# Performance work log

Hardware: AMD Instinct MI355X
Metric: run time of the kernel (lower is better)

The kernel has to match this reference:

```python
import jax, jax.numpy as jnp
import numpy as np

EPS = 1e-5


def _gcn_conv(x, src, dst, n_nodes, W, b):
    # x: [N, Fin]; src/dst: [E+N] (self-loops already appended)
    h = x @ W                                   # [N, Fout]
    deg = jnp.zeros((n_nodes,), x.dtype).at[dst].add(1.0)
    dinv = jax.lax.rsqrt(deg)                   # deg >= 1 due to self-loops
    norm = dinv[src] * dinv[dst]                # [E+N]
    msg = h[src] * norm[:, None]                # [E+N, Fout]  (gather)
    out = jax.ops.segment_sum(msg, dst, num_segments=n_nodes)  # scatter-add
    return out + b


def _bn_relu(x, gamma, beta):
    # BatchNorm over nodes (training-style batch statistics), then ReLU.
    mu = jnp.mean(x, axis=0)
    var = jnp.mean((x - mu) ** 2, axis=0)       # biased variance (torch BN)
    xn = (x - mu) * jax.lax.rsqrt(var + EPS)
    return jax.nn.relu(xn * gamma + beta)


def setup_inputs() -> dict:
    key = jax.random.key(0)
    ks = jax.random.split(key, 12)
    N, E, Fin, H, O, G = 100000, 1600000, 128, 128, 64, 128
    x = jax.random.normal(ks[0], (N, Fin), dtype=jnp.float32)
    edge_index = jax.random.randint(ks[1], (2, E), 0, N, dtype=jnp.int64)
    batch = jnp.sort(jax.random.randint(ks[2], (N,), 0, G, dtype=jnp.int64))
    s = 1.0 / np.sqrt(Fin)
    W0 = jax.random.uniform(ks[3], (Fin, H), jnp.float32, -s, s)
    b0 = jnp.zeros((H,), jnp.float32)
    g0 = jnp.ones((H,), jnp.float32)
    be0 = jnp.zeros((H,), jnp.float32)
    s2 = 1.0 / np.sqrt(H)
    W1 = jax.random.uniform(ks[4], (H, H), jnp.float32, -s2, s2)
    b1 = jnp.zeros((H,), jnp.float32)
    g1 = jnp.ones((H,), jnp.float32)
    be1 = jnp.zeros((H,), jnp.float32)
    Wout = jax.random.uniform(ks[5], (H, O), jnp.float32, -s2, s2)
    bout = jax.random.uniform(ks[6], (O,), jnp.float32, -s2, s2)
    return {"x": x, "edge_index": edge_index, "batch": batch, "num_graphs": 128,
            "W0": W0, "b0": b0, "g0": g0, "be0": be0,
            "W1": W1, "b1": b1, "g1": g1, "be1": be1,
            "Wout": Wout, "bout": bout}


def reference(x, edge_index, batch, num_graphs,
              W0, b0, g0, be0, W1, b1, g1, be1, Wout, bout):
    N = x.shape[0]
    loops = jnp.arange(N, dtype=edge_index.dtype)
    src = jnp.concatenate([edge_index[0], loops])  # add self-loops
    dst = jnp.concatenate([edge_index[1], loops])
    h = _gcn_conv(x, src, dst, N, W0, b0)
    h = _bn_relu(h, g0, be0)                       # Dropout(p=0.1) = identity in eval
    h = _gcn_conv(h, src, dst, N, W1, b1)
    h = _bn_relu(h, g1, be1)
    # global mean pool over graphs
    sums = jax.ops.segment_sum(h, batch, num_segments=num_graphs)   # [G, H]
    cnt = jax.ops.segment_sum(jnp.ones((N,), h.dtype), batch, num_segments=num_graphs)
    pooled = sums / jnp.maximum(cnt, 1.0)[:, None]
    return pooled @ Wout + bout
```

## Files before the change

### kernel.cpp

```cpp
#include <hip/hip_runtime.h>
#include <hip/hip_bf16.h>

typedef _Float16 half8_t __attribute__((ext_vector_type(8)));
typedef _Float16 half2_t __attribute__((ext_vector_type(2)));
typedef float float4_t __attribute__((ext_vector_type(4)));
typedef float float2_t __attribute__((ext_vector_type(2)));
typedef unsigned int uint4_t __attribute__((ext_vector_type(4)));


__global__ __launch_bounds__(256) void k_hist(const int* __restrict__ dst, int E, int SH,
                                              int NBK, int WG, int CH, int* __restrict__ M) {
    extern __shared__ int lh[];
    for (int i = threadIdx.x; i < NBK; i += 256) lh[i] = 0;
    __syncthreads();
    int wg = blockIdx.x;
    int e0 = wg * CH, e1 = min(E, e0 + CH);
    for (int e = e0 + threadIdx.x; e < e1; e += 256)
        atomicAdd(&lh[dst[e] >> SH], 1);
    __syncthreads();
    for (int i = threadIdx.x; i < NBK; i += 256) M[i * WG + wg] = lh[i];
}

__global__ __launch_bounds__(256) void k_colscan(int* __restrict__ M, int WG,
                                                 int* __restrict__ totals) {
    __shared__ int s[256];
    int b = blockIdx.x, t = threadIdx.x;
    int v = (t < WG) ? M[b * WG + t] : 0;
    s[t] = v;
    __syncthreads();
    for (int off = 1; off < 256; off <<= 1) {
        int u = (t >= off) ? s[t - off] : 0;
        __syncthreads();
        s[t] += u;
        __syncthreads();
    }
    if (t < WG) M[b * WG + t] = s[t] - v;
    if (t == 255) totals[b] = s[255];
}

__global__ __launch_bounds__(512) void k_bucketscan(const int* __restrict__ totals, int NBK,
                                                    int E, int* __restrict__ base) {
    __shared__ int s[512];
    int t = threadIdx.x;
    int v = (t < NBK) ? totals[t] : 0;
    s[t] = v;
    __syncthreads();
    for (int off = 1; off < 512; off <<= 1) {
        int u = (t >= off) ? s[t - off] : 0;
        __syncthreads();
        s[t] += u;
        __syncthreads();
    }
    if (t < NBK) base[t] = s[t] - v;
    if (t == 0) base[NBK] = E;
}

__global__ __launch_bounds__(256) void k_scatter(const int* __restrict__ src,
                                                 const int* __restrict__ dst, int E, int SH,
                                                 int NBK, int WG, int CH,
                                                 const int* __restrict__ M,
                                                 const int* __restrict__ base,
                                                 unsigned* __restrict__ ebuf) {
    extern __shared__ int cur[];
    int wg = blockIdx.x;
    for (int i = threadIdx.x; i < NBK; i += 256) cur[i] = base[i] + M[i * WG + wg];
    __syncthreads();
    int e0 = wg * CH, e1 = min(E, e0 + CH);
    for (int e = e0 + threadIdx.x; e < e1; e += 256) {
        int d = dst[e];
        int b = d >> SH;
        int pos = atomicAdd(&cur[b], 1);
        ebuf[pos] = (unsigned)src[e] | ((unsigned)(d - (b << SH)) << 23);
    }
}

__global__ __launch_bounds__(256) void k_cntfill(const unsigned* __restrict__ ebuf,
                                                 const int* __restrict__ base, int SH, int N,
                                                 int E, float* __restrict__ dinv,
                                                 int* __restrict__ rp, int* __restrict__ colx,
                                                 int* __restrict__ slots,
                                                 const float* __restrict__ W0,
                                                 const float* __restrict__ W1,
                                                 _Float16* __restrict__ Wt0,
                                                 _Float16* __restrict__ Wt1,
                                                 const int* __restrict__ batch, int G,
                                                 int* __restrict__ gptr,
                                                 float* __restrict__ psum,
                                                 float* __restrict__ sums,
                                                 unsigned char* __restrict__ A8) {
    __shared__ int h[512];
    __shared__ int cur[512];
    __shared__ int rs[512];
    __shared__ int lim[512];
    __shared__ int s[256];
    int b = blockIdx.x, t = threadIdx.x;

    if (b < 64) {
        int idx = b * 256 + t;
        int n = idx >> 7, k = idx & 127;
        Wt0[n * 128 + k] = (_Float16)W0[k * 128 + n];
        Wt1[n * 128 + k] = (_Float16)W1[k * 128 + n];
    } else if (b == 64) {
        if (t <= G) {
            int g = t;
            int lo = 0, hi = N;
            while (lo < hi) {
                int mid = (lo + hi) >> 1;
                if (batch[mid] < g) lo = mid + 1; else hi = mid;
            }
            gptr[g] = lo;
        }
    } else if (b < 97) {
        int i0 = (b - 65) * 512 + t;
        psum[i0] = 0.f;
        psum[i0 + 256] = 0.f;
    } else if (b == 97) {
        if (t < 256) { sums[t] = 0.f; sums[t + 256] = 0.f; }
        if (t < 32) ((unsigned*)A8)[(size_t)N * 32 + t] = 0u;
    }

    int n0 = b << SH;
    int nb = min(N - n0, 1 << SH);
    for (int i = t; i < nb; i += 256) h[i] = 0;
    __syncthreads();
    int e0 = base[b], e1 = base[b + 1];
    for (int e = e0 + t; e < e1; e += 256)
        atomicAdd(&h[ebuf[e] >> 23], 1);
    __syncthreads();
    int i0 = 2 * t, i1 = 2 * t + 1;
    int a0 = (i0 < nb) ? h[i0] : 0;
    int a1 = (i1 < nb) ? h[i1] : 0;
    int ps = a0 + a1;
    s[t] = ps;
    __syncthreads();
    for (int off = 1; off < 256; off <<= 1) {
        int u = (t >= off) ? s[t - off] : 0;
        __syncthreads();
        s[t] += u;
        __syncthreads();
    }
    int excl = s[t] - ps;
    if (i0 < nb) {
        int r0 = e0 + excl;
        cur[i0] = r0;
        rs[i0] = r0;
        lim[i0] = min(a0, 32);
        rp[n0 + i0] = r0;
        dinv[n0 + i0] = rsqrtf((float)(a0 + 1));
    }
    if (i1 < nb) {
        int r1 = e0 + excl + a0;
        cur[i1] = r1;
        rs[i1] = r1;
        lim[i1] = min(a1, 32);
        rp[n0 + i1] = r1;
        dinv[n0 + i1] = rsqrtf((float)(a1 + 1));
    }
    if (b == (int)gridDim.x - 1 && t == 0) rp[N] = E;
    __syncthreads();
    for (int e = e0 + t; e < e1; e += 256) {
        unsigned v = ebuf[e];
        int local = (int)(v >> 23);
        int srcn = (int)(v & 0x7FFFFFu);
        int pos = atomicAdd(&cur[local], 1);
        int off = pos - rs[local];
        if (slots && off < lim[local]) {
            int idx = ((off & 3) << 3) + (off >> 2);
            slots[(size_t)(n0 + local) * 32 + idx] = srcn;
        } else {
            colx[pos] = srcn;
        }
    }
}


__global__ __launch_bounds__(256) void k_gemmM(const float* __restrict__ X,
                                               const _Float16* __restrict__ Wt,
                                               const float* __restrict__ dinv,
                                               unsigned char* __restrict__ out, int N) {
    int t = threadIdx.x;
    int wv = t >> 6, lane = t & 63;
    int m = lane & 15, quad = lane >> 4;
    int rowbase = blockIdx.x * 64 + wv * 16;
    int arow = rowbase + m;
    int arowc = (arow < N) ? arow : (N - 1);
    const float* xr = X + (size_t)arowc * 128;

    float4_t acc[8];
    #pragma unroll
    for (int i = 0; i < 8; i++) acc[i] = (float4_t){0.f, 0.f, 0.f, 0.f};

    #pragma unroll
    for (int kc = 0; kc < 4; kc++) {
        int k0 = kc * 32 + quad * 8;
        float4_t xa = __builtin_nontemporal_load((const float4_t*)(xr + k0));
        float4_t xb = __builtin_nontemporal_load((const float4_t*)(xr + k0 + 4));
        half8_t a;
        #pragma unroll
        for (int j = 0; j < 4; j++) a[j] = (_Float16)xa[j];
        #pragma unroll
        for (int j = 0; j < 4; j++) a[4 + j] = (_Float16)xb[j];
        #pragma unroll
        for (int nt = 0; nt < 8; nt++) {
            half8_t b = *(const half8_t*)(Wt + (size_t)(nt * 16 + m) * 128 + k0);
            acc[nt] = __builtin_amdgcn_mfma_f32_16x16x32_f16(a, b, acc[nt], 0, 0, 0);
        }
    }

    float dv[4];
    #pragma unroll
    for (int r = 0; r < 4; r++) {
        int row = rowbase + quad * 4 + r;
        dv[r] = dinv[(row < N) ? row : (N - 1)];
    }
    #pragma unroll
    for (int r = 0; r < 4; r++) {
        int row = rowbase + quad * 4 + r;
        if (row < N) {
            unsigned char* o = out + (size_t)row * 128 + m;
            #pragma unroll
            for (int nt = 0; nt < 8; nt++) {
                float v = acc[nt][r] * dv[r];
                int pk = __builtin_amdgcn_cvt_pk_fp8_f32(v, v, 0, false);
                o[nt * 16] = (unsigned char)(pk & 0xFF);
            }
        }
    }
}

__global__ __launch_bounds__(256) void k_gemmM16(const _Float16* __restrict__ X,
                                                 const _Float16* __restrict__ Wt,
                                                 const float* __restrict__ sums,
                                                 const float* __restrict__ g,
                                                 const float* __restrict__ be,
                                                 const float* __restrict__ dinv,
                                                 unsigned char* __restrict__ out, int N) {
    __shared__ alignas(16) float ss[128];
    __shared__ alignas(16) float hh[128];
    int t = threadIdx.x;
    if (t < 128) {
        float invN = 1.0f / (float)N;
        float mu = sums[t] * invN;
        float var = fmaxf(sums[128 + t] * invN - mu * mu, 0.f);
        float sc = g[t] * rsqrtf(var + 1e-5f);
        ss[t] = sc;
        hh[t] = fmaf(-mu, sc, be[t]);
    }
    __syncthreads();

    int wv = t >> 6, lane = t & 63;
    int m = lane & 15, quad = lane >> 4;
    int rowbase = blockIdx.x * 64 + wv * 16;
    int arow = rowbase + m;
    int arowc = (arow < N) ? arow : (N - 1);
    const _Float16* xr = X + (size_t)arowc * 128;

    float4_t acc[8];
    #pragma unroll
    for (int i = 0; i < 8; i++) acc[i] = (float4_t){0.f, 0.f, 0.f, 0.f};

    #pragma unroll
    for (int kc = 0; kc < 4; kc++) {
        int k0 = kc * 32 + quad * 8;
        uint4_t xraw = __builtin_nontemporal_load((const uint4_t*)(xr + k0));
        half8_t x8 = __builtin_bit_cast(half8_t, xraw);
        float4_t sa = *(const float4_t*)(ss + k0);
        float4_t sb = *(const float4_t*)(ss + k0 + 4);
        float4_t ha = *(const float4_t*)(hh + k0);
        float4_t hb = *(const float4_t*)(hh + k0 + 4);
        half8_t a;
        #pragma unroll
        for (int j = 0; j < 4; j++)
            a[j] = (_Float16)fmaxf(fmaf((float)x8[j], sa[j], ha[j]), 0.f);
        #pragma unroll
        for (int j = 0; j < 4; j++)
            a[4 + j] = (_Float16)fmaxf(fmaf((float)x8[4 + j], sb[j], hb[j]), 0.f);
        #pragma unroll
        for (int nt = 0; nt < 8; nt++) {
            half8_t b = *(const half8_t*)(Wt + (size_t)(nt * 16 + m) * 128 + k0);
            acc[nt] = __builtin_amdgcn_mfma_f32_16x16x32_f16(a, b, acc[nt], 0, 0, 0);
        }
    }

    float dv[4];
    #pragma unroll
    for (int r = 0; r < 4; r++) {
        int row = rowbase + quad * 4 + r;
        dv[r] = dinv[(row < N) ? row : (N - 1)];
    }
    #pragma unroll
    for (int r = 0; r < 4; r++) {
        int row = rowbase + quad * 4 + r;
        if (row < N) {
            unsigned char* o = out + (size_t)row * 128 + m;
            #pragma unroll
            for (int nt = 0; nt < 8; nt++) {
                float v = acc[nt][r] * dv[r];
                int pk = __builtin_amdgcn_cvt_pk_fp8_f32(v, v, 0, false);
                o[nt * 16] = (unsigned char)(pk & 0xFF);
            }
        }
    }
}


__device__ __forceinline__ void acc8(uint2 v, float2_t* a2) {
    a2[0] += __builtin_amdgcn_cvt_pk_f32_fp8((int)v.x, false);
    a2[1] += __builtin_amdgcn_cvt_pk_f32_fp8((int)v.x, true);
    a2[2] += __builtin_amdgcn_cvt_pk_f32_fp8((int)v.y, false);
    a2[3] += __builtin_amdgcn_cvt_pk_f32_fp8((int)v.y, true);
}

__device__ __forceinline__ void f8x4(unsigned w, float* o) {
    o[0] = __builtin_amdgcn_cvt_f32_fp8((int)w, 0);
    o[1] = __builtin_amdgcn_cvt_f32_fp8((int)w, 1);
    o[2] = __builtin_amdgcn_cvt_f32_fp8((int)w, 2);
    o[3] = __builtin_amdgcn_cvt_f32_fp8((int)w, 3);
}

__global__ __launch_bounds__(256) void k_aggS8(const unsigned char* __restrict__ hs,
                                               const int* __restrict__ slots,
                                               const int* __restrict__ rp,
                                               const int* __restrict__ colx,
                                               const float* __restrict__ bias,
                                               _Float16* __restrict__ out, int N) {
    int wave = (blockIdx.x * 256 + threadIdx.x) >> 6;
    int lane = threadIdx.x & 63;
    if (wave >= N) return;
    int i = wave;
    int q = lane >> 4;
    int c8 = lane & 15;

    const int4* sl4 = (const int4*)(slots + (size_t)i * 32 + 8 * q);
    int4 sa = sl4[0];
    int k0 = rp[i], k1 = rp[i + 1];
    uint2 sw = *(const uint2*)(hs + (size_t)i * 128 + c8 * 8);
    int deg = k1 - k0;

    float2_t a2[4] = {{0.f, 0.f}, {0.f, 0.f}, {0.f, 0.f}, {0.f, 0.f}};

    {
        int jraw[4] = {sa.x, sa.y, sa.z, sa.w};
        int j[4];
        #pragma unroll
        for (int s = 0; s < 4; s++)
            j[s] = (q + 4 * s < deg) ? jraw[s] : N;
        uint2 v[4];
        #pragma unroll
        for (int s = 0; s < 4; s++)
            v[s] = *(const uint2*)(hs + (size_t)j[s] * 128 + c8 * 8);
        #pragma unroll
        for (int s = 0; s < 4; s++) acc8(v[s], a2);
    }
    if (deg > 16) {
        int4 sb = sl4[1];
        int jraw[4] = {sb.x, sb.y, sb.z, sb.w};
        int j[4];
        #pragma unroll
        for (int s = 0; s < 4; s++)
            j[s] = (16 + q + 4 * s < deg) ? jraw[s] : N;
        uint2 v[4];
        #pragma unroll
        for (int s = 0; s < 4; s++)
            v[s] = *(const uint2*)(hs + (size_t)j[s] * 128 + c8 * 8);
        #pragma unroll
        for (int s = 0; s < 4; s++) acc8(v[s], a2);
        if (deg > 32) {
            for (int k = k0 + 32 + q; k < k1; k += 4) {
                uint2 vv = *(const uint2*)(hs + (size_t)colx[k] * 128 + c8 * 8);
                acc8(vv, a2);
            }
        }
    }

    float a[8] = {a2[0].x, a2[0].y, a2[1].x, a2[1].y,
                  a2[2].x, a2[2].y, a2[3].x, a2[3].y};
    #pragma unroll
    for (int t = 0; t < 8; t++) {
        float x = a[t];
        x += __shfl_xor(x, 16);
        x += __shfl_xor(x, 32);
        a[t] = x;
    }

    if (q == 0) {
        float d = rsqrtf((float)(deg + 1));
        float4 bA = ((const float4*)bias)[2 * c8];
        float4 bB = ((const float4*)bias)[2 * c8 + 1];
        float bb[8] = {bA.x, bA.y, bA.z, bA.w, bB.x, bB.y, bB.z, bB.w};
        float sf[8];
        f8x4(sw.x, sf);
        f8x4(sw.y, sf + 4);
        half8_t o;
        #pragma unroll
        for (int t = 0; t < 8; t++)
            o[t] = (_Float16)fmaf(a[t] + sf[t], d, bb[t]);
        ((half8_t*)out)[(size_t)i * 16 + c8] = o;
    }
}

__global__ __launch_bounds__(256) void k_aggC8(const unsigned char* __restrict__ hs,
                                               const int* __restrict__ rp,
                                               const int* __restrict__ colx,
                                               const float* __restrict__ bias,
                                               _Float16* __restrict__ out, int N) {
    int wave = (blockIdx.x * 256 + threadIdx.x) >> 6;
    int lane = threadIdx.x & 63;
    if (wave >= N) return;
    int i = wave;
    int q = lane >> 4;
    int c8 = lane & 15;

    uint2 sw = *(const uint2*)(hs + (size_t)i * 128 + c8 * 8);
    int k0 = rp[i], k1 = rp[i + 1];

    float2_t a2[4] = {{0.f, 0.f}, {0.f, 0.f}, {0.f, 0.f}, {0.f, 0.f}};
    for (int k = k0 + q; k < k1; k += 4) {
        uint2 vv = *(const uint2*)(hs + (size_t)colx[k] * 128 + c8 * 8);
        acc8(vv, a2);
    }

    float a[8] = {a2[0].x, a2[0].y, a2[1].x, a2[1].y,
                  a2[2].x, a2[2].y, a2[3].x, a2[3].y};
    #pragma unroll
    for (int t = 0; t < 8; t++) {
        float x = a[t];
        x += __shfl_xor(x, 16);
        x += __shfl_xor(x, 32);
        a[t] = x;
    }

    if (q == 0) {
        float d = rsqrtf((float)(k1 - k0 + 1));
        float4 bA = ((const float4*)bias)[2 * c8];
        float4 bB = ((const float4*)bias)[2 * c8 + 1];
        float bb[8] = {bA.x, bA.y, bA.z, bA.w, bB.x, bB.y, bB.z, bB.w};
        float sf[8];
        f8x4(sw.x, sf);
        f8x4(sw.y, sf + 4);
        half8_t o;
        #pragma unroll
        for (int t = 0; t < 8; t++)
            o[t] = (_Float16)fmaf(a[t] + sf[t], d, bb[t]);
        ((half8_t*)out)[(size_t)i * 16 + c8] = o;
    }
}


__global__ __launch_bounds__(256) void k_stats(const _Float16* __restrict__ x, int N,
                                               float* __restrict__ sums) {
    int lane = threadIdx.x & 63;
    int wv = threadIdx.x >> 6;
    int gw = blockIdx.x * 4 + wv;
    int stride = gridDim.x * 4;
    const half2_t* b = (const half2_t*)x;
    float2 s = make_float2(0.f, 0.f), q = make_float2(0.f, 0.f);
    for (int i = gw; i < N; i += stride) {
        half2_t v = b[(size_t)i * 64 + lane];
        float vx = (float)v.x, vy = (float)v.y;
        s.x += vx; s.y += vy;
        q.x += vx * vx; q.y += vy * vy;
    }
    __shared__ float ls[4][128];
    __shared__ float lq[4][128];
    ls[wv][2 * lane] = s.x; ls[wv][2 * lane + 1] = s.y;
    lq[wv][2 * lane] = q.x; lq[wv][2 * lane + 1] = q.y;
    __syncthreads();
    int t = threadIdx.x;
    if (t < 128) {
        float ts = ls[0][t] + ls[1][t] + ls[2][t] + ls[3][t];
        float tq = lq[0][t] + lq[1][t] + lq[2][t] + lq[3][t];
        atomicAdd(&sums[t], ts);
        atomicAdd(&sums[128 + t], tq);
    }
}


__global__ __launch_bounds__(256) void k_pool2(const _Float16* __restrict__ x,
                                               const int* __restrict__ batch,
                                               const float* __restrict__ sums,
                                               const float* __restrict__ g2,
                                               const float* __restrict__ be2,
                                               float* __restrict__ psum, int N) {
    __shared__ alignas(8) float ss[128];
    __shared__ alignas(8) float hh[128];
    int t = threadIdx.x;
    if (t < 128) {
        float invN = 1.0f / (float)N;
        float mu = sums[t] * invN;
        float var = fmaxf(sums[128 + t] * invN - mu * mu, 0.f);
        float sc = g2[t] * rsqrtf(var + 1e-5f);
        ss[t] = sc;
        hh[t] = fmaf(-mu, sc, be2[t]);
    }
    __syncthreads();

    int nw = gridDim.x * 4;
    int w = blockIdx.x * 4 + (threadIdx.x >> 6);
    int lane = threadIdx.x & 63;
    int per = (N + nw - 1) / nw;
    int i0 = w * per, i1 = min(N, i0 + per);
    if (i0 >= i1) return;
    const half2_t* b = (const half2_t*)x;
    float2 s2 = ((const float2*)ss)[lane];
    float2 h2 = ((const float2*)hh)[lane];
    float2 acc = make_float2(0.f, 0.f);
    int g = batch[i0];
    for (int i = i0; i < i1; i++) {
        int gi = batch[i];
        if (gi != g) {
            atomicAdd(&psum[g * 128 + 2 * lane], acc.x);
            atomicAdd(&psum[g * 128 + 2 * lane + 1], acc.y);
            acc = make_float2(0.f, 0.f);
            g = gi;
        }
        half2_t v = b[(size_t)i * 64 + lane];
        acc.x += fmaxf(fmaf((float)v.x, s2.x, h2.x), 0.f);
        acc.y += fmaxf(fmaf((float)v.y, s2.y, h2.y), 0.f);
    }
    atomicAdd(&psum[g * 128 + 2 * lane], acc.x);
    atomicAdd(&psum[g * 128 + 2 * lane + 1], acc.y);
}


__global__ __launch_bounds__(64) void k_final(const float* __restrict__ psum,
                                              const int* __restrict__ gptr,
                                              const float* __restrict__ Wout,
                                              const float* __restrict__ bout,
                                              float* __restrict__ out, int O) {
    int g = blockIdx.x, o = threadIdx.x;
    int cnt = gptr[g + 1] - gptr[g];
    float inv = 1.0f / fmaxf((float)cnt, 1.f);
    float acc = 0.f;
    for (int c = 0; c < 128; c++) acc = fmaf(psum[g * 128 + c], Wout[c * O + o], acc);
    out[g * O + o] = fmaf(acc, inv, bout[o]);
}


extern "C" void kernel_launch(void* const* d_in, const int* in_sizes, int n_in,
                              void* d_out, int out_size, void* d_ws, size_t ws_size,
                              hipStream_t stream) {
    const float* x    = (const float*)d_in[0];
    const int*   edge = (const int*)d_in[1];
    const int*   batch= (const int*)d_in[2];
    const float* W0   = (const float*)d_in[4];
    const float* b0   = (const float*)d_in[5];
    const float* g0   = (const float*)d_in[6];
    const float* be0  = (const float*)d_in[7];
    const float* W1   = (const float*)d_in[8];
    const float* b1   = (const float*)d_in[9];
    const float* g1   = (const float*)d_in[10];
    const float* be1  = (const float*)d_in[11];
    const float* Wout = (const float*)d_in[12];
    const float* bout = (const float*)d_in[13];
    float* out = (float*)d_out;

    const int Hh  = in_sizes[5];
    const int Fin = in_sizes[4] / Hh;
    const int N   = in_sizes[0] / Fin;
    const int E   = in_sizes[1] / 2;
    const int O   = in_sizes[13];
    const int G   = out_size / O;
    (void)Hh; (void)n_in;

    int SH = 8;
    while (((N + (1 << SH) - 1) >> SH) > 512) SH++;
    const int NBK = (N + (1 << SH) - 1) >> SH;
    const int CH  = ((E + 255) / 256 > 8192) ? (E + 255) / 256 : 8192;
    const int WG  = (E + CH - 1) / CH;

    char* p = (char*)d_ws;
    auto alloc = [&](size_t bytes) -> void* {
        void* r = (void*)p;
        p += (bytes + 255) & ~(size_t)255;
        return r;
    };
    unsigned char* A8 = (unsigned char*)alloc((size_t)(N + 1) * 128);
    _Float16* B   = (_Float16*)alloc((size_t)N * 128 * 2);
    float* dinv   = (float*)alloc((size_t)N * 4);
    int*   rp     = (int*)alloc((size_t)(N + 1) * 4);
    int*   colx   = (int*)alloc((size_t)E * 4);
    unsigned* ebuf= (unsigned*)alloc((size_t)E * 4);
    int*   M      = (int*)alloc((size_t)NBK * WG * 4);
    int*   totals = (int*)alloc((size_t)NBK * 4);
    int*   base   = (int*)alloc((size_t)(NBK + 1) * 4);
    float* sums   = (float*)alloc(512 * 4);
    int*   gptr   = (int*)alloc((size_t)(G + 1) * 4);
    float* psum   = (float*)alloc((size_t)G * 128 * 4);
    _Float16* Wt0 = (_Float16*)alloc(128 * 128 * 2);
    _Float16* Wt1 = (_Float16*)alloc(128 * 128 * 2);
    int*   slots  = (int*)alloc((size_t)N * 32 * 4);
    bool useSlots = ((size_t)(p - (char*)d_ws) <= ws_size);
    if (!useSlots) slots = nullptr;

    const int* src = edge;
    const int* dst = edge + E;

    k_hist<<<WG, 256, NBK * 4, stream>>>(dst, E, SH, NBK, WG, CH, M);
    k_colscan<<<NBK, 256, 0, stream>>>(M, WG, totals);
    k_bucketscan<<<1, 512, 0, stream>>>(totals, NBK, E, base);
    k_scatter<<<WG, 256, NBK * 4, stream>>>(src, dst, E, SH, NBK, WG, CH, M, base, ebuf);
    k_cntfill<<<NBK, 256, 0, stream>>>(ebuf, base, SH, N, E, dinv, rp, colx, slots,
                                       W0, W1, Wt0, Wt1, batch, G, gptr, psum, sums, A8);

    k_gemmM<<<(N + 63) / 64, 256, 0, stream>>>(x, Wt0, dinv, A8, N);
    if (useSlots)
        k_aggS8<<<(N + 3) / 4, 256, 0, stream>>>(A8, slots, rp, colx, b0, B, N);
    else
        k_aggC8<<<(N + 3) / 4, 256, 0, stream>>>(A8, rp, colx, b0, B, N);
    k_stats<<<512, 256, 0, stream>>>(B, N, sums);

    k_gemmM16<<<(N + 63) / 64, 256, 0, stream>>>(B, Wt1, sums, g0, be0, dinv, A8, N);
    if (useSlots)
        k_aggS8<<<(N + 3) / 4, 256, 0, stream>>>(A8, slots, rp, colx, b1, B, N);
    else
        k_aggC8<<<(N + 3) / 4, 256, 0, stream>>>(A8, rp, colx, b1, B, N);
    k_stats<<<512, 256, 0, stream>>>(B, N, sums + 256);

    k_pool2<<<512, 256, 0, stream>>>(B, batch, sums + 256, g1, be1, psum, N);
    k_final<<<G, 64, 0, stream>>>(psum, gptr, Wout, bout, out, O);
}
```

Baseline: 400.4 us.

## Split GEMM output columns across waves so each block handles 16 rows

Both dense transform kernels now give each block 16 rows, and the four waves split the 128 output columns, two 16-column tiles per wave, where before each wave did 16 rows times all 128 columns. This launches four times as many blocks with far fewer accumulators per thread, aiming at better occupancy and latency hiding. The cost is that every wave in a block loads and converts the same A row fragment, so activation loads and the BN/ReLU prologue are repeated four times, though these likely hit in cache. Nontemporal loads are replaced with ordinary loads so the repeated reads can be served from cache.

```diff
diff --git a/kernel.cpp b/kernel.cpp
--- a/kernel.cpp
+++ b/kernel.cpp
@@ -5,7 +5,6 @@
 typedef _Float16 half2_t __attribute__((ext_vector_type(2)));
 typedef float float4_t __attribute__((ext_vector_type(4)));
 typedef float float2_t __attribute__((ext_vector_type(2)));
-typedef unsigned int uint4_t __attribute__((ext_vector_type(4)));
 
 
 __global__ __launch_bounds__(256) void k_hist(const int* __restrict__ dst, int E, int SH,
@@ -174,67 +173,63 @@
 }
 
 
-__global__ __launch_bounds__(256) void k_gemmM(const float* __restrict__ X,
+__global__ __launch_bounds__(256) void k_gemmA(const float* __restrict__ X,
                                                const _Float16* __restrict__ Wt,
                                                const float* __restrict__ dinv,
                                                unsigned char* __restrict__ out, int N) {
     int t = threadIdx.x;
     int wv = t >> 6, lane = t & 63;
     int m = lane & 15, quad = lane >> 4;
-    int rowbase = blockIdx.x * 64 + wv * 16;
+    int rowbase = blockIdx.x * 16;
     int arow = rowbase + m;
     int arowc = (arow < N) ? arow : (N - 1);
     const float* xr = X + (size_t)arowc * 128;
-
-    float4_t acc[8];
-    #pragma unroll
-    for (int i = 0; i < 8; i++) acc[i] = (float4_t){0.f, 0.f, 0.f, 0.f};
+    const _Float16* wt0 = Wt + (size_t)(wv * 2 * 16 + m) * 128;
+    const _Float16* wt1 = wt0 + (size_t)16 * 128;
+
+    float4_t acc0 = (float4_t){0.f, 0.f, 0.f, 0.f};
+    float4_t acc1 = (float4_t){0.f, 0.f, 0.f, 0.f};
 
     #pragma unroll
     for (int kc = 0; kc < 4; kc++) {
         int k0 = kc * 32 + quad * 8;
-        float4_t xa = __builtin_nontemporal_load((const float4_t*)(xr + k0));
-        float4_t xb = __builtin_nontemporal_load((const float4_t*)(xr + k0 + 4));
+        float4_t xa = *(const float4_t*)(xr + k0);
+        float4_t xb = *(const float4_t*)(xr + k0 + 4);
         half8_t a;
-        #pragma unroll
-        for (int j = 0; j < 4; j++) a[j] = (_Float16)xa[j];
-        #pragma unroll
-        for (int j = 0; j < 4; j++) a[4 + j] = (_Float16)xb[j];
-        #pragma unroll
-        for (int nt = 0; nt < 8; nt++) {
-            half8_t b = *(const half8_t*)(Wt + (size_t)(nt * 16 + m) * 128 + k0);
-            acc[nt] = __builtin_amdgcn_mfma_f32_16x16x32_f16(a, b, acc[nt], 0, 0, 0);
-        }
-    }
-
-    float dv[4];
-    #pragma unroll
-    for (int r = 0; r < 4; r++) {
-        int row = rowbase + quad * 4 + r;
-        dv[r] = dinv[(row < N) ? row : (N - 1)];
-    }
+        a[0] = (_Float16)xa[0]; a[1] = (_Float16)xa[1];
+        a[2] = (_Float16)xa[2]; a[3] = (_Float16)xa[3];
+        a[4] = (_Float16)xb[0]; a[5] = (_Float16)xb[1];
+        a[6] = (_Float16)xb[2]; a[7] = (_Float16)xb[3];
+        half8_t b0 = *(const half8_t*)(wt0 + k0);
+        half8_t b1 = *(const half8_t*)(wt1 + k0);
+        acc0 = __builtin_amdgcn_mfma_f32_16x16x32_f16(a, b0, acc0, 0, 0, 0);
+        acc1 = __builtin_amdgcn_mfma_f32_16x16x32_f16(a, b1, acc1, 0, 0, 0);
+    }
+
+    int ntb = wv * 2;
     #pragma unroll
     for (int r = 0; r < 4; r++) {
         int row = rowbase + quad * 4 + r;
         if (row < N) {
+            float dv = dinv[row];
             unsigned char* o = out + (size_t)row * 128 + m;
-            #pragma unroll
-            for (int nt = 0; nt < 8; nt++) {
-                float v = acc[nt][r] * dv[r];
-                int pk = __builtin_amdgcn_cvt_pk_fp8_f32(v, v, 0, false);
-                o[nt * 16] = (unsigned char)(pk & 0xFF);
-            }
+            float v0 = acc0[r] * dv;
+            float v1 = acc1[r] * dv;
+            int p0 = __builtin_amdgcn_cvt_pk_fp8_f32(v0, v0, 0, false);
+            int p1 = __builtin_amdgcn_cvt_pk_fp8_f32(v1, v1, 0, false);
+            o[ntb * 16]       = (unsigned char)(p0 & 0xFF);
+            o[(ntb + 1) * 16] = (unsigned char)(p1 & 0xFF);
         }
     }
 }
 
-__global__ __launch_bounds__(256) void k_gemmM16(const _Float16* __restrict__ X,
-                                                 const _Float16* __restrict__ Wt,
-                                                 const float* __restrict__ sums,
-                                                 const float* __restrict__ g,
-                                                 const float* __restrict__ be,
-                                                 const float* __restrict__ dinv,
-                                                 unsigned char* __restrict__ out, int N) {
+__global__ __launch_bounds__(256) void k_gemmB(const _Float16* __restrict__ X,
+                                               const _Float16* __restrict__ Wt,
+                                               const float* __restrict__ sums,
+                                               const float* __restrict__ g,
+                                               const float* __restrict__ be,
+                                               const float* __restrict__ dinv,
+                                               unsigned char* __restrict__ out, int N) {
     __shared__ alignas(16) float ss[128];
     __shared__ alignas(16) float hh[128];
     int t = threadIdx.x;
@@ -250,20 +245,20 @@
 
     int wv = t >> 6, lane = t & 63;
     int m = lane & 15, quad = lane >> 4;
-    int rowbase = blockIdx.x * 64 + wv * 16;
+    int rowbase = blockIdx.x * 16;
     int arow = rowbase + m;
     int arowc = (arow < N) ? arow : (N - 1);
     const _Float16* xr = X + (size_t)arowc * 128;
-
-    float4_t acc[8];
-    #pragma unroll
-    for (int i = 0; i < 8; i++) acc[i] = (float4_t){0.f, 0.f, 0.f, 0.f};
+    const _Float16* wt0 = Wt + (size_t)(wv * 2 * 16 + m) * 128;
+    const _Float16* wt1 = wt0 + (size_t)16 * 128;
+
+    float4_t acc0 = (float4_t){0.f, 0.f, 0.f, 0.f};
+    float4_t acc1 = (float4_t){0.f, 0.f, 0.f, 0.f};
 
     #pragma unroll
     for (int kc = 0; kc < 4; kc++) {
         int k0 = kc * 32 + quad * 8;
-        uint4_t xraw = __builtin_nontemporal_load((const uint4_t*)(xr + k0));
-        half8_t x8 = __builtin_bit_cast(half8_t, xraw);
+        half8_t x8 = *(const half8_t*)(xr + k0);
         float4_t sa = *(const float4_t*)(ss + k0);
         float4_t sb = *(const float4_t*)(ss + k0 + 4);
         float4_t ha = *(const float4_t*)(hh + k0);
@@ -275,30 +270,25 @@
         #pragma unroll
         for (int j = 0; j < 4; j++)
             a[4 + j] = (_Float16)fmaxf(fmaf((float)x8[4 + j], sb[j], hb[j]), 0.f);
-        #pragma unroll
-        for (int nt = 0; nt < 8; nt++) {
-            half8_t b = *(const half8_t*)(Wt + (size_t)(nt * 16 + m) * 128 + k0);
-            acc[nt] = __builtin_amdgcn_mfma_f32_16x16x32_f16(a, b, acc[nt], 0, 0, 0);
-        }
-    }
-
-    float dv[4];
-    #pragma unroll
-    for (int r = 0; r < 4; r++) {
-        int row = rowbase + quad * 4 + r;
-        dv[r] = dinv[(row < N) ? row : (N - 1)];
-    }
+        half8_t b0 = *(const half8_t*)(wt0 + k0);
+        half8_t b1 = *(const half8_t*)(wt1 + k0);
+        acc0 = __builtin_amdgcn_mfma_f32_16x16x32_f16(a, b0, acc0, 0, 0, 0);
+        acc1 = __builtin_amdgcn_mfma_f32_16x16x32_f16(a, b1, acc1, 0, 0, 0);
+    }
+
+    int ntb = wv * 2;
     #pragma unroll
     for (int r = 0; r < 4; r++) {
         int row = rowbase + quad * 4 + r;
         if (row < N) {
+            float dv = dinv[row];
             unsigned char* o = out + (size_t)row * 128 + m;
-            #pragma unroll
-            for (int nt = 0; nt < 8; nt++) {
-                float v = acc[nt][r] * dv[r];
-                int pk = __builtin_amdgcn_cvt_pk_fp8_f32(v, v, 0, false);
-                o[nt * 16] = (unsigned char)(pk & 0xFF);
-            }
+            float v0 = acc0[r] * dv;
+            float v1 = acc1[r] * dv;
+            int p0 = __builtin_amdgcn_cvt_pk_fp8_f32(v0, v0, 0, false);
+            int p1 = __builtin_amdgcn_cvt_pk_fp8_f32(v1, v1, 0, false);
+            o[ntb * 16]       = (unsigned char)(p0 & 0xFF);
+            o[(ntb + 1) * 16] = (unsigned char)(p1 & 0xFF);
         }
     }
 }
@@ -603,14 +593,14 @@
     k_cntfill<<<NBK, 256, 0, stream>>>(ebuf, base, SH, N, E, dinv, rp, colx, slots,
                                        W0, W1, Wt0, Wt1, batch, G, gptr, psum, sums, A8);
 
-    k_gemmM<<<(N + 63) / 64, 256, 0, stream>>>(x, Wt0, dinv, A8, N);
+    k_gemmA<<<(N + 15) / 16, 256, 0, stream>>>(x, Wt0, dinv, A8, N);
     if (useSlots)
         k_aggS8<<<(N + 3) / 4, 256, 0, stream>>>(A8, slots, rp, colx, b0, B, N);
     else
         k_aggC8<<<(N + 3) / 4, 256, 0, stream>>>(A8, rp, colx, b0, B, N);
     k_stats<<<512, 256, 0, stream>>>(B, N, sums);
 
-    k_gemmM16<<<(N + 63) / 64, 256, 0, stream>>>(B, Wt1, sums, g0, be0, dinv, A8, N);
+    k_gemmB<<<(N + 15) / 16, 256, 0, stream>>>(B, Wt1, sums, g0, be0, dinv, A8, N);
     if (useSlots)
         k_aggS8<<<(N + 3) / 4, 256, 0, stream>>>(A8, slots, rp, colx, b1, B, N);
     else
```

New measurement: 415.2 us. +3.7%, slower.
